# Kernel tuning notes

Measured on AMD Instinct MI355X. Metric: run time of the kernel, lower is better.

The kernel has to match this reference:

```python
import jax, jax.numpy as jnp
import numpy as np

D = 512      # latent channels (d)
K = 512      # codebook size (k)
PATCH = 8    # encoder conv kernel/stride


def _nearest_embed(z, W):
    """z: (B, D, H, W) latents; W: (D, K) codebook. Returns (quantized (B,D,H,W), argmin (B,H,W))."""
    B, d, H, Wd = z.shape
    zf = z.transpose(0, 2, 3, 1).reshape(-1, d)                      # (N, D)
    # squared L2 distances to each code: ||z||^2 - 2 z.W + ||e||^2
    d2 = (jnp.sum(zf * zf, axis=1, keepdims=True)
          - 2.0 * (zf @ W)
          + jnp.sum(W * W, axis=0))                                   # (N, K)
    idx = jnp.argmin(d2, axis=1)                                      # (N,)
    q = jnp.take(W.T, idx, axis=0)                                    # gather: (N, D)
    q = q.reshape(B, H, Wd, d).transpose(0, 3, 1, 2)
    return q, idx.reshape(B, H, Wd)


def _encode(x, enc_w, enc_b):
    z = jax.lax.conv_general_dilated(x, enc_w, window_strides=(PATCH, PATCH),
                                     padding='VALID',
                                     dimension_numbers=('NCHW', 'OIHW', 'NCHW'))
    return z + enc_b[None, :, None, None]


def _decode(z, dec_w, dec_b):
    y = jax.lax.conv_transpose(z, dec_w, strides=(PATCH, PATCH), padding='VALID',
                               dimension_numbers=('NCHW', 'IOHW', 'NCHW'))
    return y + dec_b[None, :, None, None]


def setup_inputs() -> dict:
    key = jax.random.key(0)
    k1, k2, k3, k4 = jax.random.split(key, 4)
    x = jax.random.normal(k1, (32, 3, 256, 256), dtype=jnp.float32)
    enc_w = jax.random.normal(k2, (D, 3, PATCH, PATCH), dtype=jnp.float32) * 0.02
    enc_b = jnp.zeros((D,), jnp.float32)
    dec_w = jax.random.normal(k3, (D, 3, PATCH, PATCH), dtype=jnp.float32) * 0.02  # IOHW
    dec_b = jnp.zeros((3,), jnp.float32)
    # embedding.weight.normal_(0, 0.02); torch.fmod(weight, 0.04)
    emb_w = jnp.fmod(jax.random.normal(k4, (D, K), dtype=jnp.float32) * 0.02, 0.04)
    return {"x": x, "enc_w": enc_w, "enc_b": enc_b,
            "dec_w": dec_w, "dec_b": dec_b, "emb_w": emb_w}


def reference(x, enc_w, enc_b, dec_w, dec_b, emb_w):
    z_e = _encode(x, enc_w, enc_b)                                    # (32, 512, 32, 32)
    # lookup 1: weight_sg=True (codebook grad stopped) + straight-through estimator
    q1, argmin = _nearest_embed(z_e, jax.lax.stop_gradient(emb_w))
    z_q = z_e + jax.lax.stop_gradient(q1 - z_e)
    # lookup 2: detached encoder output, grads flow to codebook via scatter-add
    emb, _ = _nearest_embed(jax.lax.stop_gradient(z_e), emb_w)
    recon = _decode(z_q, dec_w, dec_b)                                # (32, 3, 256, 256)
    return recon, z_e, emb, argmin
```

## Files before the change

kernel.cpp:

```cpp
#include <hip/hip_runtime.h>
#include <cfloat>

#define PIXB 1024
static const size_t OFF_Z = 6291456;
static const size_t OFF_E = 23068672;
static const size_t OFF_A = 39845888;

typedef __attribute__((address_space(1))) const unsigned int cg_u32;
typedef __attribute__((address_space(3))) unsigned int l_u32;
typedef _Float16 f16x8 __attribute__((ext_vector_type(8)));
typedef _Float16 f16x4 __attribute__((ext_vector_type(4)));
typedef float f32x16 __attribute__((ext_vector_type(16)));

#define SPLIT_SCALE 4096.0f
#define SPLIT_INV   (1.0f / 4096.0f)

#define GL16(srcp, dstp) __builtin_amdgcn_global_load_lds((cg_u32*)(srcp), (l_u32*)(dstp), 16, 0, 0)

__global__ __launch_bounds__(256) void k_prep(const float* __restrict__ W,
                                              const float* __restrict__ dw,
                                              const float* __restrict__ ew,
                                              _Float16* __restrict__ wq,
                                              float* __restrict__ w2,
                                              _Float16* __restrict__ aq,
                                              _Float16* __restrict__ wrow,
                                              _Float16* __restrict__ dwh,
                                              int do_aux) {
  const int t = threadIdx.x;
  const int bx = blockIdx.x;
  __shared__ float T[64][65];
  __shared__ float T2[128][65];
  if (bx < 32) {
    __shared__ float TS[32][260];
    const int cp = bx >> 4, ch = bx & 15;
#pragma unroll
    for (int i = 0; i < 32; ++i)
      TS[i][t] = W[(size_t)(ch * 32 + i) * 512 + cp * 256 + t];
    __syncthreads();
#pragma unroll
    for (int j = 0; j < 4; ++j) {
      const int u = j * 256 + t;
      const int c = u >> 2, kslot = u & 3;
      f16x8 h, l;
#pragma unroll
      for (int jj = 0; jj < 8; ++jj) {
        const float v = TS[kslot * 8 + jj][c];
        const _Float16 hh = (_Float16)v;
        h[jj] = hh;
        l[jj] = (_Float16)((v - (float)hh) * SPLIT_SCALE);
      }
      _Float16* base = wq + cp * 262144 + ch * 16384 + kslot * 2048 + c * 8;
      *(f16x8*)(base) = h;
      *(f16x8*)(base + 8192) = l;
    }
    return;
  }
  if (bx < 34) {
    const int k = (bx - 32) * 256 + t;
    float acc = 0.f;
    for (int d = 0; d < 512; ++d) { const float v = W[(size_t)d * 512 + k]; acc = fmaf(v, v, acc); }
    w2[k] = acc;
    return;
  }
  if (bx < 46) {
    const int ch = bx - 34;
#pragma unroll
    for (int cc = 0; cc < 2; ++cc) {
      const int c = cc * 256 + t;
      const float* src = ew + (size_t)c * 192 + ch * 16;
#pragma unroll
      for (int slot = 0; slot < 2; ++slot) {
        f16x8 h, l;
#pragma unroll
        for (int j = 0; j < 8; ++j) {
          const float v = src[slot * 8 + j];
          const _Float16 hh = (_Float16)v;
          h[j] = hh;
          l[j] = (_Float16)((v - (float)hh) * SPLIT_SCALE);
        }
        const int se = slot ^ ((c >> 2) & 1);
        _Float16* dst = aq + (size_t)ch * 16384 + c * 16 + se * 8;
        *(f16x8*)dst = h;
        *(f16x8*)(dst + 8192) = l;
      }
    }
    return;
  }
  if (!do_aux) return;
  if (bx < 110) {
    const int id = bx - 46;
    const int c0 = (id & 7) * 64, d0 = (id >> 3) * 64;
#pragma unroll
    for (int i = 0; i < 16; ++i) {
      const int dl = i * 4 + (t >> 6);
      T[dl][t & 63] = W[(size_t)(d0 + dl) * 512 + c0 + (t & 63)];
    }
    __syncthreads();
#pragma unroll
    for (int i = 0; i < 16; ++i) {
      const int cl = i * 4 + (t >> 6);
      const int dl = t & 63;
      wrow[(size_t)(c0 + cl) * 512 + d0 + dl] = (_Float16)T[dl][cl];
    }
    return;
  }
  {
    const int id = bx - 110;
    const int m0 = (id % 3) * 64, d0 = (id / 3) * 128;
#pragma unroll
    for (int i = 0; i < 32; ++i) {
      const int idx = i * 256 + t;
      const int dl = idx >> 6, ml = idx & 63;
      T2[dl][ml] = dw[(size_t)(d0 + dl) * 192 + m0 + ml];
    }
    __syncthreads();
#pragma unroll
    for (int i = 0; i < 32; ++i) {
      const int idx = i * 256 + t;
      const int ml = idx >> 7, dl = idx & 127;
      dwh[(size_t)(m0 + ml) * 512 + d0 + dl] = (_Float16)T2[dl][ml];
    }
  }
}

__global__ __launch_bounds__(512) void k_encmfma(const float* __restrict__ x,
                                                 const _Float16* __restrict__ aq,
                                                 const float* __restrict__ eb,
                                                 float* __restrict__ out) {
  __shared__ __align__(16) unsigned char CB[131072];
  __shared__ float ebL[512];
  const int t = threadIdx.x;
  ebL[t] = eb[t];
  const int w = t >> 6, lane = t & 63;
  const int wc = w & 3, wp = w >> 2;
  const int n0 = blockIdx.x * 64;
  const int b = n0 >> 10, pixbase = n0 & 1023;
  const int i0 = pixbase >> 5;
  const int row = lane & 31, hi = lane >> 5;

  int ab[4];
#pragma unroll
  for (int ct = 0; ct < 4; ++ct) {
    const int c = wc * 128 + ct * 32 + row;
    ab[ct] = c * 32 + ((hi ^ ((c >> 2) & 1)) << 4);
  }
  const int u = t & 255, srow = u >> 6, vsl = u & 63;
  const int csrc = vsl ^ ((vsl >> 3) & 1);
  const float* xb = x + ((size_t)b * 3 * 256 + (i0 + (srow >> 1)) * 8 + (srow & 1)) * 256 + csrc * 4;
  const int bv0 = (((2 * row) ^ ((row >> 2) & 1)) << 4);
  const int bv1 = (((2 * row + 1) ^ ((row >> 2) & 1)) << 4);
  const int brb = wp * 4096 + (wp * 2 + hi) * 1024;

  f32x16 accA[4], accB[4];
#pragma unroll
  for (int ct = 0; ct < 4; ++ct) { accA[ct] = (f32x16)(0.0f); accB[ct] = (f32x16)(0.0f); }

#define STAGE_A(chv) { const _Float16* as_ = aq + (size_t)(chv) * 16384 + t * 8;            \
    char* ad_ = (char*)CB + ((chv) % 3) * 32768 + t * 16;                                   \
    GL16(as_, ad_); GL16(as_ + 4096, ad_ + 8192);                                           \
    GL16(as_ + 8192, ad_ + 16384); GL16(as_ + 12288, ad_ + 24576); }
#define STAGE_B(chv) GL16(xb + (((chv) >> 2) * 65536 + ((chv) & 3) * 512),                  \
                          (char*)CB + 98304 + (((chv) & 3)) * 8192 + t * 16)
#define ECOMP(chv)                                                                          \
  { const char* abuf = (const char*)CB + ((chv) % 3) * 32768;                               \
    const char* bbuf = (const char*)CB + 98304 + ((chv) & 3) * 8192 + brb;                  \
    const float4 xa = *(const float4*)(bbuf + bv0);                                         \
    const float4 xc = *(const float4*)(bbuf + bv1);                                         \
    const float xs[8] = {xa.x, xa.y, xa.z, xa.w, xc.x, xc.y, xc.z, xc.w};                   \
    f16x8 Bh, Bl;                                                                           \
    _Pragma("unroll") for (int q = 0; q < 8; ++q) {                                         \
      const _Float16 hh = (_Float16)xs[q];                                                  \
      Bh[q] = hh; Bl[q] = (_Float16)((xs[q] - (float)hh) * SPLIT_SCALE); }                  \
    __builtin_amdgcn_s_setprio(1);                                                          \
    _Pragma("unroll") for (int ct_ = 0; ct_ < 4; ++ct_) {                                   \
      const f16x8 Ah = *(const f16x8*)(abuf + ab[ct_]);                                     \
      const f16x8 Al = *(const f16x8*)(abuf + 16384 + ab[ct_]);                             \
      accA[ct_] = __builtin_amdgcn_mfma_f32_32x32x16_f16(Ah, Bh, accA[ct_], 0, 0, 0);       \
      accB[ct_] = __builtin_amdgcn_mfma_f32_32x32x16_f16(Ah, Bl, accB[ct_], 0, 0, 0);       \
      accB[ct_] = __builtin_amdgcn_mfma_f32_32x32x16_f16(Al, Bh, accB[ct_], 0, 0, 0); }     \
    __builtin_amdgcn_s_setprio(0); }
#define EPHASE(chv, waitlit)                                                                \
  { asm volatile("s_waitcnt vmcnt(" #waitlit ")" ::: "memory");                             \
    __builtin_amdgcn_sched_barrier(0);                                                      \
    __builtin_amdgcn_s_barrier();                                                           \
    ECOMP(chv);                                                                             \
    __builtin_amdgcn_s_barrier(); }

  STAGE_A(0); STAGE_B(0);
  STAGE_A(1); STAGE_B(1);
  STAGE_B(2);
#pragma unroll 1
  for (int ch = 0; ch < 9; ++ch) {
    STAGE_A(ch + 2);
    STAGE_B(ch + 3);
    EPHASE(ch, 11);
  }
  STAGE_A(11);
  EPHASE(9, 10);
  EPHASE(10, 5);
  EPHASE(11, 0);
#undef STAGE_A
#undef STAGE_B
#undef ECOMP
#undef EPHASE

  const int pl = wp * 32 + row;
#pragma unroll
  for (int ct = 0; ct < 4; ++ct) {
#pragma unroll
    for (int r = 0; r < 16; ++r) {
      const int c = wc * 128 + ct * 32 + (r & 3) + ((r >> 2) << 3) + (hi << 2);
      out[OFF_Z + ((size_t)(b * 512 + c)) * 1024 + pixbase + pl] =
          fmaf(accB[ct][r], SPLIT_INV, accA[ct][r]) + ebL[c];
    }
  }
}

__global__ __launch_bounds__(512) void k_dist(const _Float16* __restrict__ wq,
                                              const float* __restrict__ Wc,
                                              const float* __restrict__ w2ws,
                                              float* __restrict__ out) {
  __shared__ __align__(16) unsigned char CB[147456];
  __shared__ float WV[512];
  __shared__ int   WI[512];
  __shared__ int   IDX[64];
  const int t = threadIdx.x;
  const int w = t >> 6, lane = t & 63;
  const int wc = w & 3, wp = w >> 2;
  const int n0 = blockIdx.x * 64;
  const int b = n0 >> 10, pixbase = n0 & 1023;
  const int row = lane & 31, hi = lane >> 5;
  const int pl = wp * 32 + row;

  int abase[2][2];
#pragma unroll
  for (int ct = 0; ct < 2; ++ct) {
    const int cl = wc * 64 + ct * 32 + row;
#pragma unroll
    for (int ks = 0; ks < 2; ++ks)
      abase[ct][ks] = (2 * ks + hi) * 4096 + cl * 16;
  }
  const int swpl = (pl ^ ((pl >> 3) & 3)) * 16;
  const int swln = (lane ^ ((lane >> 3) & 3)) * 16;
  const int twH = (w >> 1) * 1024 + swln + (w & 1) * 8;
  const float* zsrc = out + OFF_Z + ((size_t)(b * 512 + (t >> 4))) * 1024 + pixbase + (t & 15) * 4;

#define STAGE_W(cpv, chv)                                                        \
  { const _Float16* ws_ = wq + (cpv) * 262144 + (chv) * 16384 + t * 8;           \
    char* wd_ = (char*)CB + ((chv) % 3) * 32768 + t * 16;                        \
    GL16(ws_, wd_); GL16(ws_ + 4096, wd_ + 8192);                                \
    GL16(ws_ + 8192, wd_ + 16384); GL16(ws_ + 12288, wd_ + 24576); }
#define STAGE_Z(chv)                                                             \
  GL16(zsrc + (size_t)(chv) * 32768,                                             \
       (char*)CB + 98304 + ((chv) & 3) * 8192 + t * 16)
#define TRANSPOSE(chv)                                                           \
  { const char* rb_ = (const char*)CB + 98304 + ((chv) & 3) * 8192;              \
    char* sb_ = (char*)CB + 131072 + ((chv) & 1) * 8192;                         \
    f16x4 hv_, lv_;                                                              \
    _Pragma("unroll") for (int j_ = 0; j_ < 4; ++j_) {                           \
      const float f_ = *(const float*)(rb_ + (4 * w + j_) * 256 + lane * 4);     \
      const _Float16 hh_ = (_Float16)f_;                                         \
      hv_[j_] = hh_;                                                             \
      lv_[j_] = (_Float16)((f_ - (float)hh_) * SPLIT_SCALE); }                   \
    *(f16x4*)(sb_ + twH) = hv_;                                                  \
    *(f16x4*)(sb_ + 4096 + twH) = lv_; }
#define COMPUTE(chv)                                                             \
  { const char* wb_ = (const char*)CB + ((chv) % 3) * 32768;                     \
    const char* zb_ = (const char*)CB + 131072 + ((chv) & 1) * 8192;             \
    const f16x8 Bh0 = *(const f16x8*)(zb_ + hi * 1024 + swpl);                   \
    const f16x8 Bh1 = *(const f16x8*)(zb_ + (2 + hi) * 1024 + swpl);             \
    const f16x8 Bl0 = *(const f16x8*)(zb_ + 4096 + hi * 1024 + swpl);            \
    const f16x8 Bl1 = *(const f16x8*)(zb_ + 4096 + (2 + hi) * 1024 + swpl);      \
    __builtin_amdgcn_s_setprio(1);                                               \
    _Pragma("unroll")                                                            \
    for (int ct_ = 0; ct_ < 2; ++ct_) {                                          \
      const f16x8 Ah0 = *(const f16x8*)(wb_ + abase[ct_][0]);                    \
      const f16x8 Al0 = *(const f16x8*)(wb_ + 16384 + abase[ct_][0]);            \
      const f16x8 Ah1 = *(const f16x8*)(wb_ + abase[ct_][1]);                    \
      const f16x8 Al1 = *(const f16x8*)(wb_ + 16384 + abase[ct_][1]);            \
      accA[ct_] = __builtin_amdgcn_mfma_f32_32x32x16_f16(Ah0, Bh0, accA[ct_], 0, 0, 0); \
      accB[ct_] = __builtin_amdgcn_mfma_f32_32x32x16_f16(Ah0, Bl0, accB[ct_], 0, 0, 0); \
      accB[ct_] = __builtin_amdgcn_mfma_f32_32x32x16_f16(Al0, Bh0, accB[ct_], 0, 0, 0); \
      accA[ct_] = __builtin_amdgcn_mfma_f32_32x32x16_f16(Ah1, Bh1, accA[ct_], 0, 0, 0); \
      accB[ct_] = __builtin_amdgcn_mfma_f32_32x32x16_f16(Ah1, Bl1, accB[ct_], 0, 0, 0); \
      accB[ct_] = __builtin_amdgcn_mfma_f32_32x32x16_f16(Al1, Bh1, accB[ct_], 0, 0, 0); \
    }                                                                            \
    __builtin_amdgcn_s_setprio(0); }
#define LGKM0                                                                    \
  { asm volatile("s_waitcnt lgkmcnt(0)" ::: "memory");                           \
    __builtin_amdgcn_sched_barrier(0); }
#define PHASE_T(chv, waitlit)                                                    \
  { asm volatile("s_waitcnt vmcnt(" #waitlit ")" ::: "memory");                  \
    __builtin_amdgcn_sched_barrier(0);                                           \
    __builtin_amdgcn_s_barrier();                                                \
    TRANSPOSE((chv) + 1);                                                        \
    COMPUTE(chv);                                                                \
    LGKM0;                                                                       \
    __builtin_amdgcn_s_barrier(); }
#define PHASE_F(chv, waitlit)                                                    \
  { asm volatile("s_waitcnt vmcnt(" #waitlit ")" ::: "memory");                  \
    __builtin_amdgcn_sched_barrier(0);                                           \
    __builtin_amdgcn_s_barrier();                                                \
    COMPUTE(chv);                                                                \
    LGKM0;                                                                       \
    __builtin_amdgcn_s_barrier(); }

  float bv = FLT_MAX; int bi = 0x7fffffff;

#pragma unroll 1
  for (int cp = 0; cp < 2; ++cp) {
    f32x16 accA[2], accB[2];
#pragma unroll
    for (int ct = 0; ct < 2; ++ct) { accA[ct] = (f32x16)(0.0f); accB[ct] = (f32x16)(0.0f); }
    STAGE_W(cp, 0);
    STAGE_Z(0); STAGE_Z(1); STAGE_Z(2);
    STAGE_W(cp, 1);
    asm volatile("s_waitcnt vmcnt(6)" ::: "memory");
    __builtin_amdgcn_sched_barrier(0);
    __builtin_amdgcn_s_barrier();
    TRANSPOSE(0);
    LGKM0;
    __builtin_amdgcn_s_barrier();
#pragma unroll 1
    for (int ch = 0; ch < 13; ++ch) {
      STAGE_W(cp, ch + 2);
      STAGE_Z(ch + 3);
      PHASE_T(ch, 10);
    }
    STAGE_W(cp, 15);
    PHASE_T(13, 9);
    PHASE_T(14, 4);
    PHASE_F(15, 0);

#pragma unroll
    for (int ct = 0; ct < 2; ++ct) {
#pragma unroll
      for (int r = 0; r < 16; ++r) {
        const int code = cp * 256 + wc * 64 + ct * 32 +
                         ((r & 3) + ((r >> 2) << 3) + (hi << 2));
        const float zw = fmaf(accB[ct][r], SPLIT_INV, accA[ct][r]);
        const float d2 = fmaf(-2.f, zw, w2ws[code]);
        if (d2 < bv || (d2 == bv && code < bi)) { bv = d2; bi = code; }
      }
    }
  }
#undef STAGE_W
#undef STAGE_Z
#undef TRANSPOSE
#undef COMPUTE
#undef LGKM0
#undef PHASE_T
#undef PHASE_F

  WV[w * 64 + lane] = bv;
  WI[w * 64 + lane] = bi;
  __syncthreads();
  if (t < 64) {
    const int pw = t >> 5;
    float fbv = FLT_MAX; int fbi = 0x7fffffff;
#pragma unroll
    for (int wcc = 0; wcc < 4; ++wcc)
#pragma unroll
      for (int hh = 0; hh < 2; ++hh) {
        const int li = (pw * 4 + wcc) * 64 + (t & 31) + hh * 32;
        const float v = WV[li];
        const int ii = WI[li];
        if (v < fbv || (v == fbv && ii < fbi)) { fbv = v; fbi = ii; }
      }
    out[OFF_A + n0 + t] = (float)fbi;
    IDX[t] = fbi;
  }
  __syncthreads();

  const int pix = t & 63;
  const int kidx = IDX[pix];
  for (int d = t >> 6; d < 512; d += 8)
    out[OFF_E + ((size_t)(b * 512 + d)) * 1024 + pixbase + pix] = Wc[(size_t)d * 512 + kidx];
}

__global__ __launch_bounds__(512) void k_decmfma(const _Float16* __restrict__ wrow,
                                                 const _Float16* __restrict__ dwh,
                                                 const float* __restrict__ db,
                                                 float* __restrict__ out) {
  __shared__ __align__(16) _Float16 QB[2][4096];
  __shared__ int KIDX[128];
  const int t = threadIdx.x;
  const int w = t >> 6, lane = t & 63;
  const int pt = w & 3, mg = w >> 2;
  const int blk = blockIdx.x;
  const int b = blk >> 3;
  const int pixbase = (blk & 7) * 128;
  if (t < 128) KIDX[t] = (int)out[OFF_A + b * 1024 + pixbase + t];
  __syncthreads();
  const int pixS = t >> 2, slotS = t & 3;
  const _Float16* qsrc = wrow + (size_t)KIDX[pixS] * 512 + slotS * 8;
  const int ldsW = pixS * 32 + (slotS ^ ((pixS >> 1) & 3)) * 8;

  const _Float16* abp[3];
#pragma unroll
  for (int mt = 0; mt < 3; ++mt)
    abp[mt] = dwh + (size_t)((mg * 3 + mt) * 32 + (lane & 31)) * 512 + ((lane >> 5) << 3);

  const int brow = pt * 32 + (lane & 31);
  const int bsw = (brow >> 1) & 3;
  int boff[2];
#pragma unroll
  for (int ks = 0; ks < 2; ++ks)
    boff[ks] = brow * 32 + (((ks * 2 + (lane >> 5)) ^ bsw)) * 8;

  f32x16 acc[3];
#pragma unroll
  for (int mt = 0; mt < 3; ++mt) acc[mt] = (f32x16)(0.0f);
  f16x8 A[2][3][2];
  f16x8 qd[2];

  qd[0] = *(const f16x8*)(qsrc);
#pragma unroll
  for (int mt = 0; mt < 3; ++mt)
#pragma unroll
    for (int ks = 0; ks < 2; ++ks)
      A[0][mt][ks] = *(const f16x8*)(abp[mt] + ks * 16);
  *(f16x8*)&QB[0][ldsW] = qd[0];
  qd[1] = *(const f16x8*)(qsrc + 32);
  __syncthreads();

#pragma unroll
  for (int ch = 0; ch < 16; ++ch) {
    const int par = ch & 1;
    if (ch < 15) {
      *(f16x8*)&QB[par ^ 1][ldsW] = qd[(ch + 1) & 1];
#pragma unroll
      for (int mt = 0; mt < 3; ++mt)
#pragma unroll
        for (int ks = 0; ks < 2; ++ks)
          A[par ^ 1][mt][ks] = *(const f16x8*)(abp[mt] + (ch + 1) * 32 + ks * 16);
    }
    if (ch < 14) qd[ch & 1] = *(const f16x8*)(qsrc + (ch + 2) * 32);
    const f16x8 B0 = *(const f16x8*)&QB[par][boff[0]];
    const f16x8 B1 = *(const f16x8*)&QB[par][boff[1]];
#pragma unroll
    for (int mt = 0; mt < 3; ++mt) {
      acc[mt] = __builtin_amdgcn_mfma_f32_32x32x16_f16(A[par][mt][0], B0, acc[mt], 0, 0, 0);
      acc[mt] = __builtin_amdgcn_mfma_f32_32x32x16_f16(A[par][mt][1], B1, acc[mt], 0, 0, 0);
    }
    __syncthreads();
  }

  const float b0 = db[0], b1 = db[1], b2 = db[2];
  const int pix = pixbase + pt * 32 + (lane & 31);
  const int i = pix >> 5, j = pix & 31;
#pragma unroll
  for (int mt = 0; mt < 3; ++mt) {
    const int m0 = (mg * 3 + mt) * 32;
#pragma unroll
    for (int r = 0; r < 16; ++r) {
      const int m = m0 + (r & 3) + ((r >> 2) << 3) + ((lane >> 5) << 2);
      const int c = m >> 6, ki = (m >> 3) & 7, kj = m & 7;
      const float bias = (c == 0) ? b0 : ((c == 1) ? b1 : b2);
      out[(((size_t)b * 3 + c) * 256 + i * 8 + 7 - ki) * 256 + j * 8 + 7 - kj] = acc[mt][r] + bias;
    }
  }
}

__global__ __launch_bounds__(256) void k_decode(const float* __restrict__ dw,
                                                const float* __restrict__ db,
                                                float* out) {
  __shared__ __align__(16) float Qs[32][132];
  __shared__ __align__(16) float Ws3[32][68];
  const int n0 = blockIdx.x * 128;
  const int b = n0 / PIXB, pixbase = n0 % PIXB;
  const int mt = blockIdx.y;
  const int t = threadIdx.x;
  const int pg = t & 31, ck = t >> 5;
  float acc[4][8];
#pragma unroll
  for (int p = 0; p < 4; ++p)
#pragma unroll
    for (int k = 0; k < 8; ++k) acc[p][k] = 0.f;
  for (int dc = 0; dc < 16; ++dc) {
#pragma unroll
    for (int ii = 0; ii < 4; ++ii) {
      const int id = t + ii * 256;
      const int dd = id >> 5, p4 = id & 31;
      *reinterpret_cast<float4*>(&Qs[dd][p4 * 4]) =
        *reinterpret_cast<const float4*>(&out[OFF_E + ((size_t)b * 512 + dc * 32 + dd) * 1024 + pixbase + p4 * 4]);
    }
#pragma unroll
    for (int ii = 0; ii < 2; ++ii) {
      const int id = t + ii * 256;
      const int dd = id >> 4, m4 = id & 15;
      *reinterpret_cast<float4*>(&Ws3[dd][m4 * 4]) =
        *reinterpret_cast<const float4*>(&dw[(size_t)(dc * 32 + dd) * 192 + mt * 64 + m4 * 4]);
    }
    __syncthreads();
#pragma unroll
    for (int dd = 0; dd < 32; ++dd) {
      const float4 qv = *reinterpret_cast<const float4*>(&Qs[dd][pg * 4]);
      const float4 wa = *reinterpret_cast<const float4*>(&Ws3[dd][ck * 8]);
      const float4 wb = *reinterpret_cast<const float4*>(&Ws3[dd][ck * 8 + 4]);
      const float q[4] = {qv.x, qv.y, qv.z, qv.w};
      const float wv[8] = {wa.x, wa.y, wa.z, wa.w, wb.x, wb.y, wb.z, wb.w};
#pragma unroll
      for (int p = 0; p < 4; ++p)
#pragma unroll
        for (int k = 0; k < 8; ++k) acc[p][k] = fmaf(q[p], wv[k], acc[p][k]);
    }
    __syncthreads();
  }
  const int ckg = mt * 8 + ck;
  const int c = ckg >> 3, ki = ckg & 7;
  const float bias = db[c];
#pragma unroll
  for (int p = 0; p < 4; ++p) {
    const int pix = pixbase + pg * 4 + p;
    const int i = pix >> 5, j = pix & 31;
    const size_t base = (((size_t)b * 3 + c) * 256 + i * 8 + 7 - ki) * 256 + j * 8;
#pragma unroll
    for (int kj = 0; kj < 8; ++kj) out[base + 7 - kj] = acc[p][kj] + bias;
  }
}

extern "C" void kernel_launch(void* const* d_in, const int* in_sizes, int n_in,
                              void* d_out, int out_size, void* d_ws, size_t ws_size,
                              hipStream_t stream) {
  const float* x     = (const float*)d_in[0];
  const float* enc_w = (const float*)d_in[1];
  const float* enc_b = (const float*)d_in[2];
  const float* dec_w = (const float*)d_in[3];
  const float* dec_b = (const float*)d_in[4];
  const float* emb_w = (const float*)d_in[5];
  float* out = (float*)d_out;
  float* w2 = (float*)d_ws;
  _Float16* wrow = (_Float16*)((char*)d_ws + 2048);
  _Float16* dwh  = (_Float16*)((char*)d_ws + 2048 + 524288);
  const int do_aux = (ws_size >= (size_t)(2048 + 524288 + 196608)) ? 1 : 0;
  _Float16* wq  = (_Float16*)d_out;
  _Float16* aq  = (_Float16*)((char*)d_out + 2097152);

  k_prep<<<122, 256, 0, stream>>>(emb_w, dec_w, enc_w, wq, w2, aq, wrow, dwh, do_aux);
  k_encmfma<<<512, 512, 0, stream>>>(x, aq, enc_b, out);
  k_dist<<<512, 512, 0, stream>>>(wq, emb_w, w2, out);
  if (do_aux)
    k_decmfma<<<256, 512, 0, stream>>>(wrow, dwh, dec_b, out);
  else
    k_decode<<<dim3(256, 3), 256, 0, stream>>>(dec_w, dec_b, out);
}
```

Measured before the change: 197.3 us.

## Split distance kernel across codebook quarters with separate argmin merge kernel

The nearest-code search now runs one block per 64-pixel tile and per quarter of the codebook (128 codes), giving 2048 smaller blocks that use about half the LDS, instead of 512 blocks each looping over two 256-code halves. Each block writes a partial min value and index to scratch in the output buffer, and a new merge kernel reduces the four partials, writes argmin and gathers the codebook rows. The codebook fp16 split layout is reorganised into 128-code groups, and block IDs are swizzled so blocks sharing a quarter are spread out. The aim is higher occupancy and more parallelism. The cost is that each block now reloads and re-converts its z tile four times, plus an extra launch and partial-result traffic.

```diff
diff --git a/kernel.cpp b/kernel.cpp
--- a/kernel.cpp
+++ b/kernel.cpp
@@ -49,9 +49,11 @@
         h[jj] = hh;
         l[jj] = (_Float16)((v - (float)hh) * SPLIT_SCALE);
       }
-      _Float16* base = wq + cp * 262144 + ch * 16384 + kslot * 2048 + c * 8;
+      const int qg = cp * 2 + (c >> 7);
+      const int cl = c & 127;
+      _Float16* base = wq + qg * 131072 + ch * 8192 + kslot * 1024 + cl * 8;
       *(f16x8*)(base) = h;
-      *(f16x8*)(base + 8192) = l;
+      *(f16x8*)(base + 4096) = l;
     }
     return;
   }
@@ -217,45 +219,44 @@
 }
 
 __global__ __launch_bounds__(512) void k_dist(const _Float16* __restrict__ wq,
-                                              const float* __restrict__ Wc,
                                               const float* __restrict__ w2ws,
-                                              float* __restrict__ out) {
-  __shared__ __align__(16) unsigned char CB[147456];
+                                              const float* __restrict__ zin,
+                                              float* __restrict__ pv,
+                                              int* __restrict__ pi) {
+  __shared__ __align__(16) unsigned char CB[73728];
   __shared__ float WV[512];
   __shared__ int   WI[512];
-  __shared__ int   IDX[64];
   const int t = threadIdx.x;
   const int w = t >> 6, lane = t & 63;
   const int wc = w & 3, wp = w >> 2;
-  const int n0 = blockIdx.x * 64;
+  const int bid0 = blockIdx.x;
+  const int swz = (bid0 & 7) * 256 + (bid0 >> 3);
+  const int tile = swz >> 2, q = swz & 3;
+  const int n0 = tile * 64;
   const int b = n0 >> 10, pixbase = n0 & 1023;
   const int row = lane & 31, hi = lane >> 5;
   const int pl = wp * 32 + row;
 
-  int abase[2][2];
-#pragma unroll
-  for (int ct = 0; ct < 2; ++ct) {
-    const int cl = wc * 64 + ct * 32 + row;
-#pragma unroll
-    for (int ks = 0; ks < 2; ++ks)
-      abase[ct][ks] = (2 * ks + hi) * 4096 + cl * 16;
-  }
+  int abase[2];
+#pragma unroll
+  for (int ks = 0; ks < 2; ++ks)
+    abase[ks] = (2 * ks + hi) * 2048 + (wc * 32 + row) * 16;
   const int swpl = (pl ^ ((pl >> 3) & 3)) * 16;
   const int swln = (lane ^ ((lane >> 3) & 3)) * 16;
   const int twH = (w >> 1) * 1024 + swln + (w & 1) * 8;
-  const float* zsrc = out + OFF_Z + ((size_t)(b * 512 + (t >> 4))) * 1024 + pixbase + (t & 15) * 4;
-
-#define STAGE_W(cpv, chv)                                                        \
-  { const _Float16* ws_ = wq + (cpv) * 262144 + (chv) * 16384 + t * 8;           \
-    char* wd_ = (char*)CB + ((chv) % 3) * 32768 + t * 16;                        \
-    GL16(ws_, wd_); GL16(ws_ + 4096, wd_ + 8192);                                \
-    GL16(ws_ + 8192, wd_ + 16384); GL16(ws_ + 12288, wd_ + 24576); }
+  const float* zsrc = zin + OFF_Z + ((size_t)(b * 512 + (t >> 4))) * 1024 + pixbase + (t & 15) * 4;
+  const _Float16* wqb = wq + q * 131072;
+
+#define STAGE_W(chv)                                                             \
+  { const _Float16* ws_ = wqb + (chv) * 8192 + t * 8;                            \
+    char* wd_ = (char*)CB + ((chv) & 1) * 16384 + t * 16;                        \
+    GL16(ws_, wd_); GL16(ws_ + 4096, wd_ + 8192); }
 #define STAGE_Z(chv)                                                             \
   GL16(zsrc + (size_t)(chv) * 32768,                                             \
-       (char*)CB + 98304 + ((chv) & 3) * 8192 + t * 16)
+       (char*)CB + 32768 + ((chv) % 3) * 8192 + t * 16)
 #define TRANSPOSE(chv)                                                           \
-  { const char* rb_ = (const char*)CB + 98304 + ((chv) & 3) * 8192;              \
-    char* sb_ = (char*)CB + 131072 + ((chv) & 1) * 8192;                         \
+  { const char* rb_ = (const char*)CB + 32768 + ((chv) % 3) * 8192;              \
+    char* sb_ = (char*)CB + 57344 + ((chv) & 1) * 8192;                          \
     f16x4 hv_, lv_;                                                              \
     _Pragma("unroll") for (int j_ = 0; j_ < 4; ++j_) {                           \
       const float f_ = *(const float*)(rb_ + (4 * w + j_) * 256 + lane * 4);     \
@@ -265,26 +266,23 @@
     *(f16x4*)(sb_ + twH) = hv_;                                                  \
     *(f16x4*)(sb_ + 4096 + twH) = lv_; }
 #define COMPUTE(chv)                                                             \
-  { const char* wb_ = (const char*)CB + ((chv) % 3) * 32768;                     \
-    const char* zb_ = (const char*)CB + 131072 + ((chv) & 1) * 8192;             \
+  { const char* wb_ = (const char*)CB + ((chv) & 1) * 16384;                     \
+    const char* zb_ = (const char*)CB + 57344 + ((chv) & 1) * 8192;              \
     const f16x8 Bh0 = *(const f16x8*)(zb_ + hi * 1024 + swpl);                   \
     const f16x8 Bh1 = *(const f16x8*)(zb_ + (2 + hi) * 1024 + swpl);             \
     const f16x8 Bl0 = *(const f16x8*)(zb_ + 4096 + hi * 1024 + swpl);            \
     const f16x8 Bl1 = *(const f16x8*)(zb_ + 4096 + (2 + hi) * 1024 + swpl);      \
+    const f16x8 Ah0 = *(const f16x8*)(wb_ + abase[0]);                           \
+    const f16x8 Al0 = *(const f16x8*)(wb_ + 8192 + abase[0]);                    \
+    const f16x8 Ah1 = *(const f16x8*)(wb_ + abase[1]);                           \
+    const f16x8 Al1 = *(const f16x8*)(wb_ + 8192 + abase[1]);                    \
     __builtin_amdgcn_s_setprio(1);                                               \
-    _Pragma("unroll")                                                            \
-    for (int ct_ = 0; ct_ < 2; ++ct_) {                                          \
-      const f16x8 Ah0 = *(const f16x8*)(wb_ + abase[ct_][0]);                    \
-      const f16x8 Al0 = *(const f16x8*)(wb_ + 16384 + abase[ct_][0]);            \
-      const f16x8 Ah1 = *(const f16x8*)(wb_ + abase[ct_][1]);                    \
-      const f16x8 Al1 = *(const f16x8*)(wb_ + 16384 + abase[ct_][1]);            \
-      accA[ct_] = __builtin_amdgcn_mfma_f32_32x32x16_f16(Ah0, Bh0, accA[ct_], 0, 0, 0); \
-      accB[ct_] = __builtin_amdgcn_mfma_f32_32x32x16_f16(Ah0, Bl0, accB[ct_], 0, 0, 0); \
-      accB[ct_] = __builtin_amdgcn_mfma_f32_32x32x16_f16(Al0, Bh0, accB[ct_], 0, 0, 0); \
-      accA[ct_] = __builtin_amdgcn_mfma_f32_32x32x16_f16(Ah1, Bh1, accA[ct_], 0, 0, 0); \
-      accB[ct_] = __builtin_amdgcn_mfma_f32_32x32x16_f16(Ah1, Bl1, accB[ct_], 0, 0, 0); \
-      accB[ct_] = __builtin_amdgcn_mfma_f32_32x32x16_f16(Al1, Bh1, accB[ct_], 0, 0, 0); \
-    }                                                                            \
+    accA = __builtin_amdgcn_mfma_f32_32x32x16_f16(Ah0, Bh0, accA, 0, 0, 0);      \
+    accB = __builtin_amdgcn_mfma_f32_32x32x16_f16(Ah0, Bl0, accB, 0, 0, 0);      \
+    accB = __builtin_amdgcn_mfma_f32_32x32x16_f16(Al0, Bh0, accB, 0, 0, 0);      \
+    accA = __builtin_amdgcn_mfma_f32_32x32x16_f16(Ah1, Bh1, accA, 0, 0, 0);      \
+    accB = __builtin_amdgcn_mfma_f32_32x32x16_f16(Ah1, Bl1, accB, 0, 0, 0);      \
+    accB = __builtin_amdgcn_mfma_f32_32x32x16_f16(Al1, Bh1, accB, 0, 0, 0);      \
     __builtin_amdgcn_s_setprio(0); }
 #define LGKM0                                                                    \
   { asm volatile("s_waitcnt lgkmcnt(0)" ::: "memory");                           \
@@ -305,44 +303,35 @@
     LGKM0;                                                                       \
     __builtin_amdgcn_s_barrier(); }
 
+  f32x16 accA = (f32x16)(0.0f), accB = (f32x16)(0.0f);
+
+  STAGE_W(0);
+  STAGE_Z(0); STAGE_Z(1); STAGE_Z(2);
+  asm volatile("s_waitcnt vmcnt(2)" ::: "memory");
+  __builtin_amdgcn_sched_barrier(0);
+  __builtin_amdgcn_s_barrier();
+  TRANSPOSE(0);
+  LGKM0;
+  __builtin_amdgcn_s_barrier();
+#pragma unroll 1
+  for (int ch = 0; ch < 13; ++ch) {
+    STAGE_W(ch + 1);
+    STAGE_Z(ch + 3);
+    PHASE_T(ch, 4);
+  }
+  STAGE_W(14);
+  PHASE_T(13, 3);
+  STAGE_W(15);
+  PHASE_T(14, 2);
+  PHASE_F(15, 0);
+
   float bv = FLT_MAX; int bi = 0x7fffffff;
-
-#pragma unroll 1
-  for (int cp = 0; cp < 2; ++cp) {
-    f32x16 accA[2], accB[2];
-#pragma unroll
-    for (int ct = 0; ct < 2; ++ct) { accA[ct] = (f32x16)(0.0f); accB[ct] = (f32x16)(0.0f); }
-    STAGE_W(cp, 0);
-    STAGE_Z(0); STAGE_Z(1); STAGE_Z(2);
-    STAGE_W(cp, 1);
-    asm volatile("s_waitcnt vmcnt(6)" ::: "memory");
-    __builtin_amdgcn_sched_barrier(0);
-    __builtin_amdgcn_s_barrier();
-    TRANSPOSE(0);
-    LGKM0;
-    __builtin_amdgcn_s_barrier();
-#pragma unroll 1
-    for (int ch = 0; ch < 13; ++ch) {
-      STAGE_W(cp, ch + 2);
-      STAGE_Z(ch + 3);
-      PHASE_T(ch, 10);
-    }
-    STAGE_W(cp, 15);
-    PHASE_T(13, 9);
-    PHASE_T(14, 4);
-    PHASE_F(15, 0);
-
-#pragma unroll
-    for (int ct = 0; ct < 2; ++ct) {
-#pragma unroll
-      for (int r = 0; r < 16; ++r) {
-        const int code = cp * 256 + wc * 64 + ct * 32 +
-                         ((r & 3) + ((r >> 2) << 3) + (hi << 2));
-        const float zw = fmaf(accB[ct][r], SPLIT_INV, accA[ct][r]);
-        const float d2 = fmaf(-2.f, zw, w2ws[code]);
-        if (d2 < bv || (d2 == bv && code < bi)) { bv = d2; bi = code; }
-      }
-    }
+#pragma unroll
+  for (int r = 0; r < 16; ++r) {
+    const int code = (q << 7) + wc * 32 + ((r & 3) + ((r >> 2) << 3) + (hi << 2));
+    const float zw = fmaf(accB[r], SPLIT_INV, accA[r]);
+    const float d2 = fmaf(-2.f, zw, w2ws[code]);
+    if (d2 < bv || (d2 == bv && code < bi)) { bv = d2; bi = code; }
   }
 #undef STAGE_W
 #undef STAGE_Z
@@ -367,11 +356,31 @@
         const int ii = WI[li];
         if (v < fbv || (v == fbv && ii < fbi)) { fbv = v; fbi = ii; }
       }
+    pv[q * 32768 + n0 + t] = fbv;
+    pi[q * 32768 + n0 + t] = fbi;
+  }
+}
+
+__global__ __launch_bounds__(512) void k_merge(const float* __restrict__ Wc,
+                                               const float* __restrict__ pv,
+                                               const int* __restrict__ pi,
+                                               float* __restrict__ out) {
+  __shared__ int IDX[64];
+  const int t = threadIdx.x;
+  const int n0 = blockIdx.x * 64;
+  const int b = n0 >> 10, pixbase = n0 & 1023;
+  if (t < 64) {
+    float fbv = pv[n0 + t]; int fbi = pi[n0 + t];
+#pragma unroll
+    for (int q = 1; q < 4; ++q) {
+      const float v = pv[q * 32768 + n0 + t];
+      const int ii = pi[q * 32768 + n0 + t];
+      if (v < fbv || (v == fbv && ii < fbi)) { fbv = v; fbi = ii; }
+    }
     out[OFF_A + n0 + t] = (float)fbi;
     IDX[t] = fbi;
   }
   __syncthreads();
-
   const int pix = t & 63;
   const int kidx = IDX[pix];
   for (int d = t >> 6; d < 512; d += 8)
@@ -536,10 +545,13 @@
   const int do_aux = (ws_size >= (size_t)(2048 + 524288 + 196608)) ? 1 : 0;
   _Float16* wq  = (_Float16*)d_out;
   _Float16* aq  = (_Float16*)((char*)d_out + 2097152);
+  float* pv = (float*)((char*)d_out + 4194304);
+  int*   pi = (int*)((char*)d_out + 4194304 + 524288);
 
   k_prep<<<122, 256, 0, stream>>>(emb_w, dec_w, enc_w, wq, w2, aq, wrow, dwh, do_aux);
   k_encmfma<<<512, 512, 0, stream>>>(x, aq, enc_b, out);
-  k_dist<<<512, 512, 0, stream>>>(wq, emb_w, w2, out);
+  k_dist<<<2048, 512, 0, stream>>>(wq, w2, out, pv, pi);
+  k_merge<<<512, 512, 0, stream>>>(emb_w, pv, pi, out);
   if (do_aux)
     k_decmfma<<<256, 512, 0, stream>>>(wrow, dwh, dec_b, out);
   else
```

New measurement: 186.0 us, median of 3. 5.7% less time.
